# Kernel optimization log

Hardware: AMD Instinct MI355X
Metric: run time of the kernel (lower is better)

The kernel has to match this reference:

```python
import jax, jax.numpy as jnp
import numpy as np

N_FFT = 512
HOP = 128
REF_MIC = 0
B, C, T = 8, 8, 64000


def hann(n):
    # periodic Hann, like torch.hann_window
    return 0.5 - 0.5 * jnp.cos(2.0 * jnp.pi * jnp.arange(n) / n)


def stft(x, n_fft, hop, window):
    # torch.stft with center=True, reflect padding, onesided
    pad = n_fft // 2
    pads = [(0, 0)] * (x.ndim - 1) + [(pad, pad)]
    xp = jnp.pad(x, pads, mode="reflect")
    n_frames = 1 + (xp.shape[-1] - n_fft) // hop
    idx = jnp.arange(n_frames)[:, None] * hop + jnp.arange(n_fft)[None, :]
    frames = xp[..., idx] * window                  # (..., N, n_fft)
    X = jnp.fft.rfft(frames, axis=-1)               # (..., N, F)
    return jnp.swapaxes(X, -1, -2)                  # (..., F, N)


def istft(X, n_fft, hop, window):
    # torch.istft: windowed overlap-add with squared-window normalization
    pad = n_fft // 2
    Xt = jnp.swapaxes(X, -1, -2)                    # (..., N, F)
    frames = jnp.fft.irfft(Xt, n=n_fft, axis=-1) * window  # (..., N, n_fft)
    n_frames = frames.shape[-2]
    out_len = n_fft + hop * (n_frames - 1)
    idx = jnp.arange(n_frames)[:, None] * hop + jnp.arange(n_fft)[None, :]
    y = jnp.zeros(frames.shape[:-2] + (out_len,), frames.dtype).at[..., idx].add(frames)
    wsum = jnp.zeros((out_len,), frames.dtype).at[idx].add(
        jnp.broadcast_to(window ** 2, (n_frames, n_fft)))
    y = y / jnp.maximum(wsum, 1e-10)
    return y[..., pad:out_len - pad]                # undo center padding


def mwf_forward(x, w1, b1, w2, b2):
    window = hann(N_FFT).astype(x.dtype)
    X = stft(x, N_FFT, HOP, window)                 # (B, C, F, N) complex
    X = X[..., 1:, :]                               # drop DC bin -> F' = n_fft//2
    b, c, fp, n = X.shape
    # --- mask model: 2-layer MLP on |X_ref| over frequency, per frame ---
    Xref = X[..., REF_MIC, :, :]                    # (B, F', N)
    feat = jnp.abs(Xref).swapaxes(-1, -2)           # (B, N, F')
    h = jax.nn.relu(feat @ w1 + b1)                 # (B, N, H)
    m = jax.nn.sigmoid(h @ w2 + b2)                 # (B, N, 2*F')
    masks = m.reshape(b, n, 2, fp).transpose(0, 2, 3, 1)[:, None]  # (B,1,2,F',N)
    mask_t = masks[..., 0, :, :]                    # (B, 1, F', N)
    mask_n = masks[..., 1, :, :]
    # --- masked spatial covariance matrices ---
    R_tgt = jnp.einsum("bsfn,bcfn,bdfn->bsfcd", mask_t, X, X.conj())
    R_noise = jnp.einsum("bsfn,bcfn,bdfn->bsfcd", mask_n, X, X.conj())
    # --- MWF beamforming weights: (R_t + R_n)^{-1} R_t e_ref ---
    rhs = R_tgt[..., REF_MIC]                       # (B, 1, F', C)
    bf = jnp.linalg.solve(R_tgt + R_noise, rhs[..., None])[..., 0]
    Xe = jnp.einsum("bcfn,bsfc->bsfn", X, bf.conj())  # (B, 1, F', N)
    # pad DC bin back with zeros
    Xe = jnp.concatenate([jnp.zeros(Xe.shape[:-2] + (1, n), Xe.dtype), Xe], axis=-2)
    y = istft(Xe, N_FFT, HOP, window)               # (B, 1, T')
    t = x.shape[-1]
    if y.shape[-1] < t:
        y = jnp.concatenate(
            [y, jnp.zeros(y.shape[:-1] + (t - y.shape[-1],), y.dtype)], axis=-1)
    else:
        y = y[..., :t]
    return y


def setup_inputs() -> dict:
    key = jax.random.key(0)
    k1, k2, k3 = jax.random.split(key, 3)
    fp, hid = N_FFT // 2, 512
    x = jax.random.normal(k1, (B, C, T), dtype=jnp.float32)
    w1 = jax.random.normal(k2, (fp, hid), dtype=jnp.float32) * (1.0 / np.sqrt(fp))
    b1 = jnp.zeros((hid,), dtype=jnp.float32)
    w2 = jax.random.normal(k3, (hid, 2 * fp), dtype=jnp.float32) * (1.0 / np.sqrt(hid))
    b2 = jnp.zeros((2 * fp,), dtype=jnp.float32)
    return {"x": x, "w1": w1, "b1": b1, "w2": w2, "b2": b2}


def reference(x, w1, b1, w2, b2):
    return mwf_forward(x, w1, b1, w2, b2)
```

## Files before the change

### kernel.cpp

```cpp
#include <hip/hip_runtime.h>
#include <hip/hip_bf16.h>
#include <math.h>

#define NFFT 512
#define HOP  128
#define PADW 256
#define TLEN 64000
#define NF   501
#define NFP  504
#define FP   256
#define CH   8
#define BATCH 8
#define HID  512
#define MROWS (BATCH * NF)
#define FPB  8
#define NGRP 63
#define NSTG 4

#define S2C 0.70710678118654752f

typedef short bf16x8 __attribute__((ext_vector_type(8)));
typedef float f32x4 __attribute__((ext_vector_type(4)));

__device__ __forceinline__ unsigned short f2bf(float v) {
    __hip_bfloat16 hb = __float2bfloat16(v);
    return *reinterpret_cast<unsigned short*>(&hb);
}

__device__ __forceinline__ float2 cadd(float2 a, float2 b) { return make_float2(a.x + b.x, a.y + b.y); }
__device__ __forceinline__ float2 csub(float2 a, float2 b) { return make_float2(a.x - b.x, a.y - b.y); }
__device__ __forceinline__ float2 cmul(float2 a, float2 b) { return make_float2(a.x * b.x - a.y * b.y, a.x * b.y + a.y * b.x); }
__device__ __forceinline__ float2 mulnegi(float2 a) { return make_float2(a.y, -a.x); }

__device__ __forceinline__ void dft8(const float2 u[8], float2 v[8]) {
    float2 a0 = cadd(u[0], u[4]), a1 = cadd(u[1], u[5]), a2 = cadd(u[2], u[6]), a3 = cadd(u[3], u[7]);
    float2 b0 = csub(u[0], u[4]), b1 = csub(u[1], u[5]), b2 = csub(u[2], u[6]), b3 = csub(u[3], u[7]);
    float2 c0 = cadd(a0, a2), c1 = csub(a0, a2), c2 = cadd(a1, a3), c3 = csub(a1, a3);
    v[0] = cadd(c0, c2); v[4] = csub(c0, c2);
    float2 nic3 = mulnegi(c3);
    v[2] = cadd(c1, nic3); v[6] = csub(c1, nic3);
    float2 d1 = make_float2(S2C * (b1.x + b1.y), S2C * (b1.y - b1.x));
    float2 d2 = mulnegi(b2);
    float2 d3 = make_float2(S2C * (b3.y - b3.x), -S2C * (b3.x + b3.y));
    float2 e0 = cadd(b0, d2), e1 = csub(b0, d2), e2 = cadd(d1, d3), e3 = csub(d1, d3);
    v[1] = cadd(e0, e2); v[5] = csub(e0, e2);
    float2 nie3 = mulnegi(e3);
    v[3] = cadd(e1, nie3); v[7] = csub(e1, nie3);
}

__device__ __forceinline__ int refl(int j) {
    j = (j < 0) ? -j : j;
    j = (j >= TLEN) ? 2 * (TLEN - 1) - j : j;
    return j;
}

__global__ __launch_bounds__(256) void k_prep(const float* __restrict__ w1,
                                              const float* __restrict__ w2,
                                              float* __restrict__ tw,
                                              unsigned short* __restrict__ wt1,
                                              unsigned short* __restrict__ wt2) {
    __shared__ float tile[32][33];
    int bid = blockIdx.x;
    if (bid == 384) {
        #pragma unroll
        for (int r = 0; r < 2; ++r) {
            int e = threadIdx.x + 256 * r;
            float ang = (float)(2.0 * M_PI * (double)e / 512.0);
            tw[e] = 0.5f - 0.5f * cosf(ang);
        }
        return;
    }
    const float* w; unsigned short* wt; int K, lb;
    if (bid < 128) { w = w1; wt = wt1; K = 256; lb = bid; }
    else           { w = w2; wt = wt2; K = 512; lb = bid - 128; }
    int nt = lb & 15, kt = lb >> 4;
    int tx = threadIdx.x & 31, ty = threadIdx.x >> 5;
    #pragma unroll
    for (int r = 0; r < 4; ++r)
        tile[ty + 8 * r][tx] = w[(size_t)(kt * 32 + ty + 8 * r) * HID + nt * 32 + tx];
    __syncthreads();
    #pragma unroll
    for (int r = 0; r < 4; ++r)
        wt[(size_t)(nt * 32 + ty + 8 * r) * K + kt * 32 + tx] = f2bf(tile[tx][ty + 8 * r]);
}

#define A_S 580
#define B_S 544
__global__ __launch_bounds__(256, 4) void k_stft(const float* __restrict__ x,
                                                 const float* __restrict__ tw,
                                                 float2* __restrict__ X,
                                                 unsigned short* __restrict__ featbf) {
    __shared__ float2 Abuf[4 * A_S];
    __shared__ float2 Bbuf[4 * B_S];
    __shared__ float2 Twd[512];
    int blk = blockIdx.x;
    int g = blk % NGRP;
    int bc = blk / NGRP;
    int c = bc % CH, b = bc / CH;
    int m0 = g * FPB;
    int tid = threadIdx.x;
    const float* xp = x + (size_t)(b * CH + c) * TLEN;

    #pragma unroll
    for (int r = 0; r < 2; ++r) {
        int e = tid + 256 * r;
        float se, ce;
        sincosf((float)e * (float)(2.0 * M_PI / 512.0), &se, &ce);
        Twd[e] = make_float2(ce, -se);
    }

    float* xs = (float*)Bbuf;
    int base = m0 * HOP - PADW;
    #pragma unroll
    for (int r = 0; r < 6; ++r) {
        int i = r * 256 + tid;
        xs[i] = xp[refl(base + i)];
    }
    __syncthreads();

    #pragma unroll
    for (int r = 0; r < 8; ++r) {
        int flat = r * 256 + tid;
        int sig = flat >> 9, t = flat & 511;
        float w = tw[t];
        Abuf[sig * A_S + t] = make_float2(xs[2 * sig * 128 + t] * w,
                                          xs[(2 * sig + 1) * 128 + t] * w);
    }
    __syncthreads();

    int sig = tid >> 6, dft = tid & 63;
    float2 u[8], v[8];

    {
        const float2* Az = &Abuf[sig * A_S];
        float2* Bu = &Bbuf[sig * B_S];
        #pragma unroll
        for (int a = 0; a < 8; ++a) u[a] = Az[64 * a + dft];
        dft8(u, v);
        #pragma unroll
        for (int k0 = 0; k0 < 8; ++k0) Bu[k0 * 68 + dft] = v[k0];
    }
    __syncthreads();

    {
        int k0 = dft >> 3, cd = dft & 7;
        const float2* Bu = &Bbuf[sig * B_S];
        float2* Au = &Abuf[sig * A_S];
        #pragma unroll
        for (int bb = 0; bb < 8; ++bb) u[bb] = Bu[k0 * 68 + 8 * bb + cd];
        #pragma unroll
        for (int bb = 1; bb < 8; ++bb) u[bb] = cmul(u[bb], Twd[(8 * bb * k0) & 511]);
        dft8(u, v);
        #pragma unroll
        for (int k1 = 0; k1 < 8; ++k1) Au[(8 * k0 + k1) * 9 + cd] = v[k1];
    }
    __syncthreads();

    {
        int k0 = dft >> 3, k1 = dft & 7;
        int kk = k0 + 8 * k1;
        const float2* Au = &Abuf[sig * A_S];
        float2* Bz = &Bbuf[sig * B_S];
        #pragma unroll
        for (int cd = 0; cd < 8; ++cd) u[cd] = Au[dft * 9 + cd];
        #pragma unroll
        for (int cd = 1; cd < 8; ++cd) u[cd] = cmul(u[cd], Twd[(cd * kk) & 511]);
        dft8(u, v);
        #pragma unroll
        for (int k2 = 0; k2 < 8; ++k2) Bz[kk + 64 * k2] = v[k2];
    }
    __syncthreads();

    {
        int kp = tid;
        int k = kp + 1;
        #pragma unroll
        for (int s = 0; s < 4; ++s) {
            float2 z1 = Bbuf[s * B_S + k];
            float2 z2 = Bbuf[s * B_S + (512 - k)];
            float Ar = 0.5f * (z1.x + z2.x);
            float Ai = 0.5f * (z1.y - z2.y);
            float Br = 0.5f * (z1.y + z2.y);
            float Bi = 0.5f * (z2.x - z1.x);
            int ma = m0 + 2 * s, mb_ = ma + 1;
            if (ma < NF) {
                X[((size_t)(b * NF + ma) * CH + c) * FP + kp] = make_float2(Ar, Ai);
                if (c == 0) featbf[((size_t)b * NF + ma) * FP + kp] = f2bf(sqrtf(Ar * Ar + Ai * Ai));
            }
            if (mb_ < NF) {
                X[((size_t)(b * NF + mb_) * CH + c) * FP + kp] = make_float2(Br, Bi);
                if (c == 0) featbf[((size_t)b * NF + mb_) * FP + kp] = f2bf(sqrtf(Br * Br + Bi * Bi));
            }
        }
    }
}

template<int K, int ACT>
__global__ __launch_bounds__(256) void k_mfma_mlp(const unsigned short* __restrict__ Abf,
                                                  const unsigned short* __restrict__ Wt,
                                                  const float* __restrict__ bias,
                                                  float* __restrict__ outf,
                                                  unsigned short* __restrict__ outbf,
                                                  int M) {
    __shared__ unsigned short Al[64][40];
    __shared__ unsigned short Bl[128][40];
    int bid = blockIdx.x;
    int nt = bid & 3, mt = bid >> 2;
    int m0 = mt * 64, n0 = nt * 128;
    int tid = threadIdx.x;
    int wid = tid >> 6, lane = tid & 63;
    int wm = wid >> 1, wn = wid & 1;
    int lr = lane & 15, lk = (lane >> 4) * 8;

    f32x4 acc[2][4] = {};

    int arow = tid >> 2, ak = (tid & 3) * 8;
    for (int k0 = 0; k0 < K; k0 += 32) {
        int garow = m0 + arow; if (garow > M - 1) garow = M - 1;
        float4 av = *(const float4*)&Abf[(size_t)garow * K + k0 + ak];
        int s0 = tid, s1 = tid + 256;
        float4 bv0 = *(const float4*)&Wt[(size_t)(n0 + (s0 >> 2)) * K + k0 + (s0 & 3) * 8];
        float4 bv1 = *(const float4*)&Wt[(size_t)(n0 + (s1 >> 2)) * K + k0 + (s1 & 3) * 8];
        if (k0 > 0) __syncthreads();
        *(float4*)&Al[arow][ak] = av;
        *(float4*)&Bl[s0 >> 2][(s0 & 3) * 8] = bv0;
        *(float4*)&Bl[s1 >> 2][(s1 & 3) * 8] = bv1;
        __syncthreads();
        bf16x8 af[2], bfr[4];
        af[0] = *(const bf16x8*)&Al[wm * 32 + lr][lk];
        af[1] = *(const bf16x8*)&Al[wm * 32 + 16 + lr][lk];
        #pragma unroll
        for (int nf = 0; nf < 4; ++nf)
            bfr[nf] = *(const bf16x8*)&Bl[wn * 64 + nf * 16 + lr][lk];
        #pragma unroll
        for (int mf = 0; mf < 2; ++mf)
            #pragma unroll
            for (int nf = 0; nf < 4; ++nf)
                acc[mf][nf] = __builtin_amdgcn_mfma_f32_16x16x32_bf16(af[mf], bfr[nf], acc[mf][nf], 0, 0, 0);
    }

    int rbase = (lane >> 4) * 4;
    #pragma unroll
    for (int mf = 0; mf < 2; ++mf) {
        #pragma unroll
        for (int nf = 0; nf < 4; ++nf) {
            int n = n0 + wn * 64 + nf * 16 + lr;
            float bj = bias[n];
            #pragma unroll
            for (int r = 0; r < 4; ++r) {
                int m = m0 + wm * 32 + mf * 16 + rbase + r;
                if (m < M) {
                    float vv = acc[mf][nf][r] + bj;
                    if (ACT == 0) {
                        outbf[(size_t)m * HID + n] = f2bf(fmaxf(vv, 0.f));
                    } else {
                        outf[(size_t)m * HID + n] = 1.f / (1.f + expf(-vv));
                    }
                }
            }
        }
    }
}

__global__ __launch_bounds__(512) void k_cov(const float2* __restrict__ X,
                                             const float* __restrict__ mo,
                                             float2* __restrict__ part, int cck) {
    int nc = blockIdx.x, ftile = blockIdx.y, b = blockIdx.z;
    int tid = threadIdx.x;
    int c = tid >> 6;
    int ft = tid & 63;
    int f = ftile * 64 + ft;
    int n0 = nc * cck;
    int n1 = n0 + cck; if (n1 > NF) n1 = NF;

    __shared__ float2 vbuf[2][NSTG][CH][64];

    float ar[8], ai[8];
    #pragma unroll
    for (int d = 0; d < 8; ++d) { ar[d] = 0.f; ai[d] = 0.f; }
    float rr = 0.f, ri = 0.f;

    const float2* Xb = X + (size_t)b * NF * CH * FP;
    const float* mb = mo + (size_t)b * NF * HID;

    #pragma unroll
    for (int r = 0; r < NSTG; ++r) {
        int n = n0 + r;
        if (n < n1) vbuf[0][r][c][ft] = Xb[(size_t)(n * CH + c) * FP + f];
    }
    __syncthreads();
    int cur = 0;
    for (int nb = n0; nb < n1; nb += NSTG) {
        int nbn = nb + NSTG;
        float2 nx[NSTG];
        #pragma unroll
        for (int r = 0; r < NSTG; ++r) {
            int n = nbn + r;
            if (n < n1) nx[r] = Xb[(size_t)(n * CH + c) * FP + f];
        }
        float mts[NSTG], mns[NSTG];
        #pragma unroll
        for (int r = 0; r < NSTG; ++r) {
            int n = nb + r;
            if (n < n1) {
                mts[r] = mb[(size_t)n * HID + f];
                mns[r] = mb[(size_t)n * HID + FP + f];
            }
        }
        #pragma unroll
        for (int r = 0; r < NSTG; ++r) {
            int n = nb + r;
            if (n < n1) {
                float mt = mts[r], mn = mns[r];
                float w = mt + mn;
                float2 xc = vbuf[cur][r][c][ft];
                #pragma unroll
                for (int d = 0; d < 8; ++d) {
                    float2 xd = vbuf[cur][r][d][ft];
                    float pr = xc.x * xd.x + xc.y * xd.y;
                    float pi = xc.y * xd.x - xc.x * xd.y;
                    ar[d] += w * pr; ai[d] += w * pi;
                    if (d == 0) { rr += mt * pr; ri += mt * pi; }
                }
            }
        }
        if (nbn < n1) {
            #pragma unroll
            for (int r = 0; r < NSTG; ++r) {
                int n = nbn + r;
                if (n < n1) vbuf[cur ^ 1][r][c][ft] = nx[r];
            }
        }
        __syncthreads();
        cur ^= 1;
    }
    float2* pp = part + (((size_t)nc * BATCH + b) * FP + f) * 72;
    #pragma unroll
    for (int d = 0; d < 8; ++d)
        pp[c * 8 + d] = make_float2(ar[d], ai[d]);
    pp[64 + c] = make_float2(rr, ri);
}

__global__ __launch_bounds__(512) void k_cov_solve2(const float2* __restrict__ part,
                                                    float2* __restrict__ wc, int ncnt) {
    int blk = blockIdx.x;
    int fg = blk & 31;
    int b = blk >> 5;
    int tid = threadIdx.x;
    int c = tid >> 6, d = (tid >> 3) & 7, fl = tid & 7;
    int f = fg * 8 + fl;
    float ar = 0.f, ai = 0.f, rr = 0.f, ri = 0.f;
    const float2* pb = part + ((size_t)b * FP + f) * 72;
    for (int nc = 0; nc < ncnt; ++nc) {
        const float2* p = pb + (size_t)nc * BATCH * FP * 72;
        float2 v = p[c * 8 + d];
        ar += v.x; ai += v.y;
        if (d == 0) { float2 u = p[64 + c]; rr += u.x; ri += u.y; }
    }
    __shared__ float2 Am[8][73];
    __shared__ float2 rh[8][8];
    __shared__ float2 sl[8][9];
    Am[fl][c * 9 + d] = make_float2(ar, ai);
    if (d == 0) rh[fl][c] = make_float2(rr, ri);
    __syncthreads();
    if (tid < 8) {
        int ln = tid;
        float2* A = Am[ln];
        float2* r = rh[ln];
        float2* sol = sl[ln];
        for (int kk = 0; kk < 8; ++kk) {
            float2 pp = A[kk * 9 + kk];
            float ip = 1.f / (pp.x * pp.x + pp.y * pp.y);
            float invr = pp.x * ip, invi = -pp.y * ip;
            for (int i = kk + 1; i < 8; ++i) {
                float2 aik = A[i * 9 + kk];
                float fr2 = aik.x * invr - aik.y * invi;
                float fi2 = aik.x * invi + aik.y * invr;
                for (int jj = kk; jj < 8; ++jj) {
                    float2 ak = A[kk * 9 + jj];
                    A[i * 9 + jj].x -= fr2 * ak.x - fi2 * ak.y;
                    A[i * 9 + jj].y -= fr2 * ak.y + fi2 * ak.x;
                }
                r[i].x -= fr2 * r[kk].x - fi2 * r[kk].y;
                r[i].y -= fr2 * r[kk].y + fi2 * r[kk].x;
            }
        }
        for (int kk = 7; kk >= 0; --kk) {
            float sr = r[kk].x, si = r[kk].y;
            for (int jj = kk + 1; jj < 8; ++jj) {
                float2 ak = A[kk * 9 + jj];
                float2 xj = sol[jj];
                sr -= ak.x * xj.x - ak.y * xj.y;
                si -= ak.x * xj.y + ak.y * xj.x;
            }
            float2 pp = A[kk * 9 + kk];
            float ip = 1.f / (pp.x * pp.x + pp.y * pp.y);
            sol[kk].x = (sr * pp.x + si * pp.y) * ip;
            sol[kk].y = (si * pp.x - sr * pp.y) * ip;
        }
        for (int cc = 0; cc < 8; ++cc)
            wc[((size_t)b * CH + cc) * FP + fg * 8 + ln] = make_float2(sol[cc].x, -sol[cc].y);
    }
}

__global__ __launch_bounds__(512) void k_istft_bf(const float2* __restrict__ X,
                                                  const float2* __restrict__ wc,
                                                  float* __restrict__ yfr) {
    __shared__ float2 Zp[4 * 512];
    __shared__ float2 Gl[16 * 32 * 5];
    int blk = blockIdx.x;
    int g = blk % NGRP, b = blk / NGRP;
    int m0 = g * FPB;
    int tid = threadIdx.x;

    if (tid < 4) Zp[tid * 512] = make_float2(0.f, 0.f);
    const float2* Xb0 = X + (size_t)b * NF * CH * FP;
    const float2* wcb = wc + (size_t)b * CH * FP;
    #pragma unroll
    for (int half = 0; half < 2; ++half) {
        int i = half * 512 + tid;
        int sig = i >> 8, kp = i & 255;
        int ma = m0 + 2 * sig, mb_ = ma + 1;
        float2 Xa = make_float2(0.f, 0.f), Xb = make_float2(0.f, 0.f);
        if (ma < NF) {
            #pragma unroll
            for (int c = 0; c < 8; ++c) {
                float2 xv = Xb0[(size_t)(ma * CH + c) * FP + kp];
                float2 wv = wcb[c * FP + kp];
                Xa.x += xv.x * wv.x - xv.y * wv.y;
                Xa.y += xv.x * wv.y + xv.y * wv.x;
            }
        }
        if (mb_ < NF) {
            #pragma unroll
            for (int c = 0; c < 8; ++c) {
                float2 xv = Xb0[(size_t)(mb_ * CH + c) * FP + kp];
                float2 wv = wcb[c * FP + kp];
                Xb.x += xv.x * wv.x - xv.y * wv.y;
                Xb.y += xv.x * wv.y + xv.y * wv.x;
            }
        }
        int k = kp + 1;
        if (k == 256) {
            Zp[sig * 512 + 256] = make_float2(Xa.x, Xb.x);
        } else {
            Zp[sig * 512 + k]       = make_float2(Xa.x - Xb.y, Xa.y + Xb.x);
            Zp[sig * 512 + 512 - k] = make_float2(Xa.x + Xb.y, Xb.x - Xa.y);
        }
    }
    __syncthreads();

    {
        int k1 = tid >> 5, tau = tid & 31;
        float sa, ca;
        sincosf((float)tau * (float)(2.0 * M_PI / 32.0), &sa, &ca);
        float stepc = ca, steps = sa;
        float gr[4], gi[4];
        #pragma unroll
        for (int s = 0; s < 4; ++s) { gr[s] = 0.f; gi[s] = 0.f; }
        float cr = 1.f, ci = 0.f;
        #pragma unroll 4
        for (int k2 = 0; k2 < 32; ++k2) {
            int k = k1 + 16 * k2;
            #pragma unroll
            for (int s = 0; s < 4; ++s) {
                float2 z = Zp[s * 512 + k];
                gr[s] += z.x * cr - z.y * ci;
                gi[s] += z.x * ci + z.y * cr;
            }
            float ncr = cr * stepc - ci * steps;
            ci = cr * steps + ci * stepc;
            cr = ncr;
        }
        #pragma unroll
        for (int s = 0; s < 4; ++s)
            Gl[(k1 * 32 + tau) * 5 + s] = make_float2(gr[s], gi[s]);
    }
    __syncthreads();

    int t = tid;
    int tau = t & 31;
    float sa2, ca2;
    sincosf((float)t * (float)(2.0 * M_PI / 512.0), &sa2, &ca2);
    float stepc = ca2, steps = sa2;
    float accr[4], acci[4];
    #pragma unroll
    for (int s = 0; s < 4; ++s) { accr[s] = 0.f; acci[s] = 0.f; }
    float cr = 1.f, ci = 0.f;
    #pragma unroll 4
    for (int k1 = 0; k1 < 16; ++k1) {
        #pragma unroll
        for (int s = 0; s < 4; ++s) {
            float2 gv = Gl[(k1 * 32 + tau) * 5 + s];
            accr[s] += gv.x * cr - gv.y * ci;
            acci[s] += gv.x * ci + gv.y * cr;
        }
        float ncr = cr * stepc - ci * steps;
        ci = cr * steps + ci * stepc;
        cr = ncr;
    }
    float wv = (0.5f - 0.5f * ca2) * (1.f / 512.f);
    #pragma unroll
    for (int s = 0; s < 4; ++s) {
        int ma = m0 + 2 * s, mb_ = ma + 1;
        if (ma < NF)  yfr[((size_t)b * NFP + ma) * 512 + t] = accr[s] * wv;
        if (mb_ < NF) yfr[((size_t)b * NFP + mb_) * 512 + t] = acci[s] * wv;
    }
}

__global__ __launch_bounds__(256) void k_out(const float* __restrict__ yfr,
                                             float* __restrict__ out) {
    int i = blockIdx.x * blockDim.x + threadIdx.x;
    if (i >= BATCH * TLEN) return;
    int b = i / TLEN;
    int t = i - b * TLEN;
    int p = t + PADW;
    int q = p & 127;
    int m0 = p >> 7;
    float sq, cq;
    sincosf((float)q * (float)(2.0 * M_PI / 512.0), &sq, &cq);
    float w4[4] = {0.5f - 0.5f * cq, 0.5f + 0.5f * sq, 0.5f + 0.5f * cq, 0.5f - 0.5f * sq};
    float val = 0.f, wsum = 0.f;
    const float* yb = yfr + (size_t)b * NFP * 512;
    #pragma unroll
    for (int dm = 0; dm < 4; ++dm) {
        int mm = m0 - dm;
        if (mm >= 0 && mm < NF) {
            val += yb[(size_t)mm * 512 + q + 128 * dm];
            wsum += w4[dm] * w4[dm];
        }
    }
    out[i] = val / fmaxf(wsum, 1e-10f);
}

extern "C" void kernel_launch(void* const* d_in, const int* in_sizes, int n_in,
                              void* d_out, int out_size, void* d_ws, size_t ws_size,
                              hipStream_t stream) {
    const float* x  = (const float*)d_in[0];
    const float* w1 = (const float*)d_in[1];
    const float* b1 = (const float*)d_in[2];
    const float* w2 = (const float*)d_in[3];
    const float* b2 = (const float*)d_in[4];

    float* ws = (float*)d_ws;
    size_t off = 0;
    float*  tw    = ws + off; off += 512;
    float2* X     = (float2*)(ws + off); off += (size_t)BATCH * FP * NF * CH * 2;
    float*  mo    = ws + off; off += (size_t)BATCH * NF * HID;
    float2* wc    = (float2*)(ws + off); off += (size_t)BATCH * FP * CH * 2;
    float*  yfr   = ws + off; off += (size_t)BATCH * NFP * 512;
    unsigned short* featbf = (unsigned short*)(ws + off); off += (size_t)MROWS * FP / 2;
    unsigned short* hbf    = (unsigned short*)(ws + off); off += (size_t)MROWS * HID / 2;
    unsigned short* wt1bf  = (unsigned short*)(ws + off); off += (size_t)HID * FP / 2;
    unsigned short* wt2bf  = (unsigned short*)(ws + off); off += (size_t)HID * HID / 2;
    float2* part  = (float2*)(ws + off);

    int cnck = 8, cck = 63;
    size_t need16 = (off + (size_t)16 * BATCH * FP * 72 * 2) * sizeof(float);
    if (ws_size >= need16) { cnck = 16; cck = 32; }

    k_prep<<<385, 256, 0, stream>>>(w1, w2, tw, wt1bf, wt2bf);
    k_stft<<<BATCH * CH * NGRP, 256, 0, stream>>>(x, tw, X, featbf);
    k_mfma_mlp<FP, 0><<<63 * 4, 256, 0, stream>>>(featbf, wt1bf, b1, mo, hbf, MROWS);
    k_mfma_mlp<HID, 1><<<63 * 4, 256, 0, stream>>>(hbf, wt2bf, b2, mo, hbf, MROWS);
    k_cov<<<dim3(cnck, 4, BATCH), 512, 0, stream>>>(X, mo, part, cck);
    k_cov_solve2<<<BATCH * 32, 512, 0, stream>>>(part, wc, cnck);
    k_istft_bf<<<BATCH * NGRP, 512, 0, stream>>>(X, wc, yfr);
    k_out<<<(BATCH * TLEN + 255) / 256, 256, 0, stream>>>(yfr, (float*)d_out);
}
```

Baseline: 123.7 us.

## Store STFT spectrum and mask outputs in bf16 to halve memory traffic

The complex STFT tensor X, which is written once and read by both the covariance and beamforming kernels, is now stored as bf16 pairs instead of float2. The sigmoid mask output is also written as bf16 into its own buffer instead of fp32. Both changes cut global memory traffic in the bandwidth-bound cov and istft stages. The cost is reduced precision in the covariance accumulation and the beamformer output, which could push results past the accuracy tolerance.

```diff
diff --git a/kernel.cpp b/kernel.cpp
--- a/kernel.cpp
+++ b/kernel.cpp
@@ -26,6 +26,14 @@
     __hip_bfloat16 hb = __float2bfloat16(v);
     return *reinterpret_cast<unsigned short*>(&hb);
 }
+__device__ __forceinline__ float bf2f(unsigned short u) {
+    unsigned int t = ((unsigned int)u) << 16;
+    float f;
+    __builtin_memcpy(&f, &t, 4);
+    return f;
+}
+__device__ __forceinline__ float2 bf2c(ushort2 v) { return make_float2(bf2f(v.x), bf2f(v.y)); }
+__device__ __forceinline__ ushort2 c2bf(float2 v) { ushort2 o; o.x = f2bf(v.x); o.y = f2bf(v.y); return o; }
 
 __device__ __forceinline__ float2 cadd(float2 a, float2 b) { return make_float2(a.x + b.x, a.y + b.y); }
 __device__ __forceinline__ float2 csub(float2 a, float2 b) { return make_float2(a.x - b.x, a.y - b.y); }
@@ -88,7 +96,7 @@
 #define B_S 544
 __global__ __launch_bounds__(256, 4) void k_stft(const float* __restrict__ x,
                                                  const float* __restrict__ tw,
-                                                 float2* __restrict__ X,
+                                                 ushort2* __restrict__ X,
                                                  unsigned short* __restrict__ featbf) {
     __shared__ float2 Abuf[4 * A_S];
     __shared__ float2 Bbuf[4 * B_S];
@@ -184,11 +192,11 @@
             float Bi = 0.5f * (z2.x - z1.x);
             int ma = m0 + 2 * s, mb_ = ma + 1;
             if (ma < NF) {
-                X[((size_t)(b * NF + ma) * CH + c) * FP + kp] = make_float2(Ar, Ai);
+                X[((size_t)(b * NF + ma) * CH + c) * FP + kp] = c2bf(make_float2(Ar, Ai));
                 if (c == 0) featbf[((size_t)b * NF + ma) * FP + kp] = f2bf(sqrtf(Ar * Ar + Ai * Ai));
             }
             if (mb_ < NF) {
-                X[((size_t)(b * NF + mb_) * CH + c) * FP + kp] = make_float2(Br, Bi);
+                X[((size_t)(b * NF + mb_) * CH + c) * FP + kp] = c2bf(make_float2(Br, Bi));
                 if (c == 0) featbf[((size_t)b * NF + mb_) * FP + kp] = f2bf(sqrtf(Br * Br + Bi * Bi));
             }
         }
@@ -199,7 +207,6 @@
 __global__ __launch_bounds__(256) void k_mfma_mlp(const unsigned short* __restrict__ Abf,
                                                   const unsigned short* __restrict__ Wt,
                                                   const float* __restrict__ bias,
-                                                  float* __restrict__ outf,
                                                   unsigned short* __restrict__ outbf,
                                                   int M) {
     __shared__ unsigned short Al[64][40];
@@ -251,19 +258,16 @@
                 int m = m0 + wm * 32 + mf * 16 + rbase + r;
                 if (m < M) {
                     float vv = acc[mf][nf][r] + bj;
-                    if (ACT == 0) {
-                        outbf[(size_t)m * HID + n] = f2bf(fmaxf(vv, 0.f));
-                    } else {
-                        outf[(size_t)m * HID + n] = 1.f / (1.f + expf(-vv));
-                    }
+                    float o = (ACT == 0) ? fmaxf(vv, 0.f) : 1.f / (1.f + expf(-vv));
+                    outbf[(size_t)m * HID + n] = f2bf(o);
                 }
             }
         }
     }
 }
 
-__global__ __launch_bounds__(512) void k_cov(const float2* __restrict__ X,
-                                             const float* __restrict__ mo,
+__global__ __launch_bounds__(512) void k_cov(const ushort2* __restrict__ X,
+                                             const unsigned short* __restrict__ mo,
                                              float2* __restrict__ part, int cck) {
     int nc = blockIdx.x, ftile = blockIdx.y, b = blockIdx.z;
     int tid = threadIdx.x;
@@ -280,19 +284,19 @@
     for (int d = 0; d < 8; ++d) { ar[d] = 0.f; ai[d] = 0.f; }
     float rr = 0.f, ri = 0.f;
 
-    const float2* Xb = X + (size_t)b * NF * CH * FP;
-    const float* mb = mo + (size_t)b * NF * HID;
+    const ushort2* Xb = X + (size_t)b * NF * CH * FP;
+    const unsigned short* mb = mo + (size_t)b * NF * HID;
 
     #pragma unroll
     for (int r = 0; r < NSTG; ++r) {
         int n = n0 + r;
-        if (n < n1) vbuf[0][r][c][ft] = Xb[(size_t)(n * CH + c) * FP + f];
+        if (n < n1) vbuf[0][r][c][ft] = bf2c(Xb[(size_t)(n * CH + c) * FP + f]);
     }
     __syncthreads();
     int cur = 0;
     for (int nb = n0; nb < n1; nb += NSTG) {
         int nbn = nb + NSTG;
-        float2 nx[NSTG];
+        ushort2 nx[NSTG];
         #pragma unroll
         for (int r = 0; r < NSTG; ++r) {
             int n = nbn + r;
@@ -303,8 +307,8 @@
         for (int r = 0; r < NSTG; ++r) {
             int n = nb + r;
             if (n < n1) {
-                mts[r] = mb[(size_t)n * HID + f];
-                mns[r] = mb[(size_t)n * HID + FP + f];
+                mts[r] = bf2f(mb[(size_t)n * HID + f]);
+                mns[r] = bf2f(mb[(size_t)n * HID + FP + f]);
             }
         }
         #pragma unroll
@@ -328,7 +332,7 @@
             #pragma unroll
             for (int r = 0; r < NSTG; ++r) {
                 int n = nbn + r;
-                if (n < n1) vbuf[cur ^ 1][r][c][ft] = nx[r];
+                if (n < n1) vbuf[cur ^ 1][r][c][ft] = bf2c(nx[r]);
             }
         }
         __syncthreads();
@@ -403,7 +407,7 @@
     }
 }
 
-__global__ __launch_bounds__(512) void k_istft_bf(const float2* __restrict__ X,
+__global__ __launch_bounds__(512) void k_istft_bf(const ushort2* __restrict__ X,
                                                   const float2* __restrict__ wc,
                                                   float* __restrict__ yfr) {
     __shared__ float2 Zp[4 * 512];
@@ -414,7 +418,7 @@
     int tid = threadIdx.x;
 
     if (tid < 4) Zp[tid * 512] = make_float2(0.f, 0.f);
-    const float2* Xb0 = X + (size_t)b * NF * CH * FP;
+    const ushort2* Xb0 = X + (size_t)b * NF * CH * FP;
     const float2* wcb = wc + (size_t)b * CH * FP;
     #pragma unroll
     for (int half = 0; half < 2; ++half) {
@@ -425,7 +429,7 @@
         if (ma < NF) {
             #pragma unroll
             for (int c = 0; c < 8; ++c) {
-                float2 xv = Xb0[(size_t)(ma * CH + c) * FP + kp];
+                float2 xv = bf2c(Xb0[(size_t)(ma * CH + c) * FP + kp]);
                 float2 wv = wcb[c * FP + kp];
                 Xa.x += xv.x * wv.x - xv.y * wv.y;
                 Xa.y += xv.x * wv.y + xv.y * wv.x;
@@ -434,7 +438,7 @@
         if (mb_ < NF) {
             #pragma unroll
             for (int c = 0; c < 8; ++c) {
-                float2 xv = Xb0[(size_t)(mb_ * CH + c) * FP + kp];
+                float2 xv = bf2c(Xb0[(size_t)(mb_ * CH + c) * FP + kp]);
                 float2 wv = wcb[c * FP + kp];
                 Xb.x += xv.x * wv.x - xv.y * wv.y;
                 Xb.y += xv.x * wv.y + xv.y * wv.x;
@@ -545,25 +549,25 @@
     float* ws = (float*)d_ws;
     size_t off = 0;
     float*  tw    = ws + off; off += 512;
-    float2* X     = (float2*)(ws + off); off += (size_t)BATCH * FP * NF * CH * 2;
-    float*  mo    = ws + off; off += (size_t)BATCH * NF * HID;
+    ushort2* X    = (ushort2*)(ws + off); off += (size_t)BATCH * NF * CH * FP;
     float2* wc    = (float2*)(ws + off); off += (size_t)BATCH * FP * CH * 2;
     float*  yfr   = ws + off; off += (size_t)BATCH * NFP * 512;
     unsigned short* featbf = (unsigned short*)(ws + off); off += (size_t)MROWS * FP / 2;
     unsigned short* hbf    = (unsigned short*)(ws + off); off += (size_t)MROWS * HID / 2;
+    unsigned short* mobf   = (unsigned short*)(ws + off); off += (size_t)MROWS * HID / 2;
     unsigned short* wt1bf  = (unsigned short*)(ws + off); off += (size_t)HID * FP / 2;
     unsigned short* wt2bf  = (unsigned short*)(ws + off); off += (size_t)HID * HID / 2;
     float2* part  = (float2*)(ws + off);
 
     int cnck = 8, cck = 63;
-    size_t need16 = (off + (size_t)16 * BATCH * FP * 72 * 2) * sizeof(float);
+    size_t need16 = (off + (size_t)16 * BATCH * FP * 72 * 4) * sizeof(float);
     if (ws_size >= need16) { cnck = 16; cck = 32; }
 
     k_prep<<<385, 256, 0, stream>>>(w1, w2, tw, wt1bf, wt2bf);
     k_stft<<<BATCH * CH * NGRP, 256, 0, stream>>>(x, tw, X, featbf);
-    k_mfma_mlp<FP, 0><<<63 * 4, 256, 0, stream>>>(featbf, wt1bf, b1, mo, hbf, MROWS);
-    k_mfma_mlp<HID, 1><<<63 * 4, 256, 0, stream>>>(hbf, wt2bf, b2, mo, hbf, MROWS);
-    k_cov<<<dim3(cnck, 4, BATCH), 512, 0, stream>>>(X, mo, part, cck);
+    k_mfma_mlp<FP, 0><<<63 * 4, 256, 0, stream>>>(featbf, wt1bf, b1, hbf, MROWS);
+    k_mfma_mlp<HID, 1><<<63 * 4, 256, 0, stream>>>(hbf, wt2bf, b2, mobf, MROWS);
+    k_cov<<<dim3(cnck, 4, BATCH), 512, 0, stream>>>(X, mobf, part, cck);
     k_cov_solve2<<<BATCH * 32, 512, 0, stream>>>(part, wc, cnck);
     k_istft_bf<<<BATCH * NGRP, 512, 0, stream>>>(X, wc, yfr);
     k_out<<<(BATCH * TLEN + 255) / 256, 256, 0, stream>>>(yfr, (float*)d_out);
```

Result: no change. 123.4 us (-0.2%).
